# Kernel optimization log

Measured on AMD Instinct MI355X. Metric: run time of the kernel, lower is better.

## Reference

```python
import jax, jax.numpy as jnp
import numpy as np


def _lstm_dir(x, w_ih, w_hh, b_ih, b_hh, reverse):
    # x: [B, L, D]; w_ih: [4H, D]; w_hh: [4H, H]; PyTorch gate order i,f,g,o
    B = x.shape[0]
    H = w_hh.shape[1]
    h0 = jnp.zeros((B, H), x.dtype)

    def cell(carry, x_t):
        h, c = carry
        z = x_t @ w_ih.T + h @ w_hh.T + b_ih + b_hh
        i, f, g, o = jnp.split(z, 4, axis=-1)
        c = jax.nn.sigmoid(f) * c + jax.nn.sigmoid(i) * jnp.tanh(g)
        h = jax.nn.sigmoid(o) * jnp.tanh(c)
        return (h, c), h

    _, hs = jax.lax.scan(cell, (h0, h0), jnp.swapaxes(x, 0, 1), reverse=reverse)
    return jnp.swapaxes(hs, 0, 1)  # [B, L, H]


def setup_inputs() -> dict:
    key = jax.random.key(0)
    ks = jax.random.split(key, 16)
    B, L, V, D, H, E, A = 32, 128, 30000, 300, 128, 34, 36
    s = 0.05
    rn = lambda k, shape: jax.random.normal(k, shape, jnp.float32) * s
    return {
        "input_ids": jax.random.randint(ks[0], (B, L), 0, V),
        "emb": rn(ks[1], (V, D)),
        "w_ih_f": rn(ks[2], (4 * H, D)), "w_hh_f": rn(ks[3], (4 * H, H)),
        "b_ih_f": rn(ks[4], (4 * H,)), "b_hh_f": rn(ks[5], (4 * H,)),
        "w_ih_b": rn(ks[6], (4 * H, D)), "w_hh_b": rn(ks[7], (4 * H, H)),
        "b_ih_b": rn(ks[8], (4 * H,)), "b_hh_b": rn(ks[9], (4 * H,)),
        "event_w": rn(ks[10], (E, 2 * H)), "event_b": rn(ks[11], (E,)),
        "arg_w": rn(ks[12], (A, 4 * H + E - 1)), "arg_b": rn(ks[13], (A,)),
    }


def reference(input_ids, emb, w_ih_f, w_hh_f, b_ih_f, b_hh_f,
              w_ih_b, w_hh_b, b_ih_b, b_hh_b,
              event_w, event_b, arg_w, arg_b):
    # Eval mode: dropout is identity. No labels -> return (event_logits, arguments_logits).
    B, L = input_ids.shape
    E = event_b.shape[0]
    x = emb[input_ids]  # [B, L, D]
    h_f = _lstm_dir(x, w_ih_f, w_hh_f, b_ih_f, b_hh_f, False)
    h_b = _lstm_dir(x, w_ih_b, w_hh_b, b_ih_b, b_hh_b, True)
    hidden = jnp.concatenate([h_f, h_b], axis=-1)  # [B, L, 2H]
    col_range = jnp.arange(E - 1)
    g0 = jnp.zeros((B, L, E - 1), hidden.dtype)  # running g_trg_arg memory

    def step(g, h_i):  # h_i: [B, 2H] = trigger hidden state at timestep i
        ev_logit = h_i @ event_w.T + event_b  # [B, E]
        ev_pred = jnp.argmax(ev_logit, axis=-1)  # [B]
        trig = jnp.broadcast_to(h_i[:, None, :], hidden.shape)  # [B, L, 2H]
        ah = jnp.concatenate([hidden, trig, g], axis=-1)  # [B, L, 4H+E-1]
        arg_logit = ah @ arg_w.T + arg_b  # [B, L, A]
        arg_pred = jnp.argmax(arg_logit, axis=-1)  # [B, L]
        # Vectorized update_g_trg_arg: for batch items with ev_pred>0, set
        # column (ev_pred-1) to 1 wherever arg_pred>0, else keep previous value.
        mask_ev = ev_pred > 0  # [B]
        col = jnp.where(mask_ev, ev_pred - 1, 0)  # [B]
        onehot = (col[:, None] == col_range[None, :]) & mask_ev[:, None]  # [B, E-1]
        cond = onehot[:, None, :] & (arg_pred[:, :, None] > 0)  # [B, L, E-1]
        g = jnp.where(cond, jnp.ones((), g.dtype), g)
        return g, (ev_logit, arg_logit)

    _, (ev_logits, arg_logits) = jax.lax.scan(step, g0, jnp.swapaxes(hidden, 0, 1))
    event_logits = jnp.swapaxes(ev_logits, 0, 1)  # [B, L, E]
    arguments_logits = jnp.swapaxes(arg_logits, 0, 1)  # [B, L, L, A]
    return event_logits, arguments_logits
```

## Files before the change

### kernel.cpp

```cpp
#include <hip/hip_runtime.h>
#include <hip/hip_bf16.h>
#include <stdint.h>

#define B_  32
#define L_  128
#define D_  300
#define DP_ 304
#define H_  128
#define G_  512
#define E_  34
#define A_  36
#define M_  4096
#define NC_ 106
#define NCP 112
#define CH_ 8
#define NCH 16
#define LCH 8
#define NCHK (L_ / LCH)
#define BH_ 4

typedef float f2 __attribute__((ext_vector_type(2)));

__device__ __forceinline__ float sigf(float x){ return 1.0f / (1.0f + expf(-x)); }

__device__ __forceinline__ void bar_lds(){
    asm volatile("s_waitcnt lgkmcnt(0)" ::: "memory");
    __builtin_amdgcn_s_barrier();
    __builtin_amdgcn_sched_barrier(0);
}

__global__ void k_prep1(const float* __restrict__ wihf, const float* __restrict__ wihb,
                        float* __restrict__ WT){
    int k = blockIdx.x;
    int d = blockIdx.y;
    int n = threadIdx.x;
    const float* w = d ? wihb : wihf;
    WT[((size_t)d * DP_ + k) * G_ + n] = (k < D_) ? w[(size_t)n * D_ + k] : 0.0f;
}

__global__ void k_prep2(const float* __restrict__ evw, const float* __restrict__ evb,
                        const float* __restrict__ argw, const float* __restrict__ argb,
                        float* __restrict__ WcatT, float* __restrict__ biasv){
    int k = blockIdx.x;
    int n = threadIdx.x;
    if (n >= NCP) return;
    float v = 0.0f;
    if (n < E_)       v = evw[(size_t)n * 256 + k];
    else if (n < 70)  v = argw[(size_t)(n - 34) * 545 + k];
    else if (n < NC_) v = argw[(size_t)(n - 70) * 545 + 256 + k];
    WcatT[(size_t)k * NCP + n] = v;
    if (k == 0){
        float bv = 0.0f;
        if (n < E_) bv = evb[n];
        else if (n < 70) bv = argb[n - 34];
        biasv[n] = bv;
    }
}

__launch_bounds__(256)
__global__ void k_gemm1(const int* __restrict__ ids, const float* __restrict__ emb,
                        const float* __restrict__ WT,
                        const float* __restrict__ bihf, const float* __restrict__ bhhf,
                        const float* __restrict__ bihb, const float* __restrict__ bhhb,
                        float* __restrict__ XW){
    __shared__ __align__(16) float xs[DP_][8];
    int d  = blockIdx.y;
    int m0 = blockIdx.x * 8;
    int tid = threadIdx.x;
    for (int idx = tid; idx < 8 * DP_; idx += 256){
        int r = idx / DP_, k = idx % DP_;
        int id = ids[m0 + r];
        xs[k][r] = (k < D_) ? emb[(size_t)id * D_ + k] : 0.0f;
    }
    __syncthreads();
    int n0 = tid, n1 = tid + 256;
    const float* w0 = WT + (size_t)d * DP_ * G_ + n0;
    const float* w1 = WT + (size_t)d * DP_ * G_ + n1;
    const float4* xs4 = (const float4*)xs;
    float acc0[8] = {}, acc1[8] = {};
    #pragma unroll 2
    for (int k = 0; k < D_; k++){
        float wv0 = w0[(size_t)k * G_];
        float wv1 = w1[(size_t)k * G_];
        float4 xA = xs4[k * 2], xB = xs4[k * 2 + 1];
        acc0[0] += xA.x * wv0; acc0[1] += xA.y * wv0;
        acc0[2] += xA.z * wv0; acc0[3] += xA.w * wv0;
        acc0[4] += xB.x * wv0; acc0[5] += xB.y * wv0;
        acc0[6] += xB.z * wv0; acc0[7] += xB.w * wv0;
        acc1[0] += xA.x * wv1; acc1[1] += xA.y * wv1;
        acc1[2] += xA.z * wv1; acc1[3] += xA.w * wv1;
        acc1[4] += xB.x * wv1; acc1[5] += xB.y * wv1;
        acc1[6] += xB.z * wv1; acc1[7] += xB.w * wv1;
    }
    float bias0 = d ? (bihb[n0] + bhhb[n0]) : (bihf[n0] + bhhf[n0]);
    float bias1 = d ? (bihb[n1] + bhhb[n1]) : (bihf[n1] + bhhf[n1]);
    for (int r = 0; r < 8; r++){
        XW[((size_t)d * M_ + m0 + r) * G_ + n0] = acc0[r] + bias0;
        XW[((size_t)d * M_ + m0 + r) * G_ + n1] = acc1[r] + bias1;
    }
}

#define PF(XR, CHI)                                                             \
{                                                                               \
    if ((CHI) < NCHK){                                                          \
        _Pragma("unroll")                                                       \
        for (int j = 0; j < LCH; j++){                                          \
            int s_ = (CHI) * LCH + j;                                           \
            int t_ = d ? (L_ - 1 - s_) : s_;                                    \
            XR[j] = xwn[(size_t)t_ * G_];                                       \
        }                                                                       \
    }                                                                           \
}

#define STEP8(XR, CHI)                                                          \
{                                                                               \
    _Pragma("unroll")                                                           \
    for (int j = 0; j < LCH; j++){                                              \
        int s_ = (CHI) * LCH + j;                                               \
        f2 a01 = {0.f, 0.f}, a23 = {0.f, 0.f};                                  \
        const float4* hc = (const float4*)hbuf;                                 \
        _Pragma("unroll")                                                       \
        for (int q = 0; q < 32; q++){                                           \
            float4 hv = hc[q];                                                  \
            f2 h01 = {hv.x, hv.y}, h23 = {hv.z, hv.w};                          \
            a01 = __builtin_elementwise_fma(wp[2*q],   h01, a01);               \
            a23 = __builtin_elementwise_fma(wp[2*q+1], h23, a23);               \
        }                                                                       \
        float z = XR[j] + ((a01.x + a01.y) + (a23.x + a23.y));                  \
        float v = gate_g ? tanhf(z) : sigf(z);                                  \
        zbuf[n] = v;                                                            \
        bar_lds();                                                              \
        if (n < H_){                                                            \
            float F = zbuf[H_ + n], G = zbuf[2*H_ + n], O = zbuf[3*H_ + n];     \
            c = F * c + v * G;                                                  \
            float h = O * tanhf(c);                                             \
            hbuf[n] = h;                                                        \
            hist[(size_t)(s_) * H_ + n] = h;                                    \
        }                                                                       \
        bar_lds();                                                              \
    }                                                                           \
}

__launch_bounds__(512, 2)
__global__ void k_lstm(const float* __restrict__ XW, const float* __restrict__ whhf,
                       const float* __restrict__ whhb, float* __restrict__ Hid){
    __shared__ __align__(16) float hbuf[H_];
    __shared__ float zbuf[G_];
    __shared__ __align__(16) float hist[L_ * H_];
    int bid = blockIdx.x;
    int d = bid >> 5, b = bid & 31;
    int n = threadIdx.x;
    bool gate_g = ((n >> 7) == 2);
    const float* whh = d ? whhb : whhf;
    const f2* wr2 = (const f2*)(whh + (size_t)n * H_);
    f2 wp[64];
    #pragma unroll
    for (int q = 0; q < 64; q++) wp[q] = wr2[q];
    float c = 0.0f;
    if (n < H_) hbuf[n] = 0.0f;
    __syncthreads();
    const float* xwn = XW + ((size_t)d * M_ + (size_t)b * L_) * G_ + n;
    float xA[LCH], xB[LCH];
    PF(xA, 0)
    #pragma unroll 1
    for (int cp = 0; cp < NCHK / 2; cp++){
        PF(xB, 2 * cp + 1)
        STEP8(xA, 2 * cp)
        PF(xA, 2 * cp + 2)
        STEP8(xB, 2 * cp + 1)
    }
    const float4* hist4 = (const float4*)hist;
    #pragma unroll
    for (int q = 0; q < 8; q++){
        int idx = n + q * 512;
        int sl = idx >> 5, n4 = idx & 31;
        int t_ = d ? (L_ - 1 - sl) : sl;
        *(float4*)(Hid + ((size_t)b * L_ + t_) * 256 + d * H_ + n4 * 4) =
            hist4[(size_t)sl * 32 + n4];
    }
}

__launch_bounds__(128)
__global__ void k_heads2(const float* __restrict__ Hid, const float* __restrict__ WcatT,
                         const float* __restrict__ biasv,
                         float* __restrict__ out0, float* __restrict__ Base,
                         float* __restrict__ T2, int* __restrict__ Evcol){
    __shared__ __align__(16) float hsT[256][BH_];
    __shared__ float outs[BH_][NCP];
    int m0 = blockIdx.x * BH_;
    int tid = threadIdx.x;
    #pragma unroll
    for (int r = 0; r < BH_; r++){
        hsT[tid][r]       = Hid[(size_t)(m0 + r) * 256 + tid];
        hsT[tid + 128][r] = Hid[(size_t)(m0 + r) * 256 + 128 + tid];
    }
    __syncthreads();
    if (tid < NC_){
        float acc[BH_] = {};
        const float* wc = WcatT + tid;
        for (int k = 0; k < 256; k++){
            float wv = wc[(size_t)k * NCP];
            float4 h4 = *(const float4*)&hsT[k][0];
            acc[0] += h4.x * wv;
            acc[1] += h4.y * wv;
            acc[2] += h4.z * wv;
            acc[3] += h4.w * wv;
        }
        float bv = biasv[tid];
        #pragma unroll
        for (int r = 0; r < BH_; r++) outs[r][tid] = acc[r] + bv;
    }
    __syncthreads();
    for (int idx = tid; idx < BH_ * E_; idx += 128){
        int r = idx / E_, e = idx % E_;
        out0[(size_t)(m0 + r) * E_ + e] = outs[r][e];
    }
    for (int idx = tid; idx < BH_ * A_; idx += 128){
        int r = idx / A_, a = idx % A_;
        Base[(size_t)(m0 + r) * A_ + a] = outs[r][34 + a];
        T2[(size_t)(m0 + r) * A_ + a]   = outs[r][70 + a];
    }
    if (tid < BH_){
        float best = outs[tid][0]; int bi = 0;
        for (int e = 1; e < E_; e++){
            float v = outs[tid][e];
            if (v > best){ best = v; bi = e; }
        }
        Evcol[m0 + tid] = bi - 1;
    }
}

__launch_bounds__(128)
__global__ void k_scan1(const float* __restrict__ Base, const float* __restrict__ T2,
                        const int* __restrict__ Evcol, const float* __restrict__ argw,
                        float* __restrict__ Snap, uint64_t* __restrict__ MaskSnap){
    __shared__ float t2s[L_ * A_];
    __shared__ float wgs[33 * A_];
    __shared__ int   evc[L_];
    int b = blockIdx.x;
    int l = threadIdx.x;
    for (int idx = l; idx < L_ * A_; idx += 128)
        t2s[idx] = T2[(size_t)b * L_ * A_ + idx];
    for (int idx = l; idx < 33 * A_; idx += 128){
        int c = idx / A_, a = idx % A_;
        wgs[idx] = argw[(size_t)a * 545 + 512 + c];
    }
    evc[l] = Evcol[b * L_ + l];
    __syncthreads();
    float bg[A_];
    {
        const float* bp = Base + ((size_t)b * L_ + l) * A_;
        #pragma unroll
        for (int a = 0; a < A_; a++) bg[a] = bp[a];
    }
    uint64_t mask = 0;
    #pragma unroll 1
    for (int i = 0; i < L_; i++){
        if ((i & (CH_ - 1)) == 0){
            int ch = i >> 3;
            float* sp = Snap + (((size_t)b * NCH + ch) * L_ + l) * A_;
            #pragma unroll
            for (int a = 0; a < A_; a++) sp[a] = bg[a];
            MaskSnap[((size_t)b * NCH + ch) * L_ + l] = mask;
        }
        const float* tr = t2s + i * A_;
        float lg0 = bg[0] + tr[0];
        float m1  = bg[1] + tr[1];
        #pragma unroll
        for (int a = 2; a < A_; a++) m1 = fmaxf(m1, bg[a] + tr[a]);
        bool apos = m1 > lg0;
        int cc = evc[i];
        if (cc >= 0 && apos && !((mask >> cc) & 1ull)){
            mask |= 1ull << cc;
            const float* wc = wgs + cc * A_;
            #pragma unroll
            for (int a = 0; a < A_; a++) bg[a] += wc[a];
        }
    }
}

__launch_bounds__(128)
__global__ void k_scan2(const float* __restrict__ T2, const int* __restrict__ Evcol,
                        const float* __restrict__ argw,
                        const float* __restrict__ Snap, const uint64_t* __restrict__ MaskSnap,
                        float* __restrict__ argout){
    __shared__ float t2s[CH_ * A_];
    __shared__ float wgs[33 * A_];
    __shared__ int   evc[CH_];
    __shared__ float stg[L_ * 37];
    int ch = blockIdx.x;
    int b  = blockIdx.y;
    int l  = threadIdx.x;
    int i0 = ch * CH_;
    for (int idx = l; idx < CH_ * A_; idx += 128)
        t2s[idx] = T2[((size_t)b * L_ + i0) * A_ + idx];
    for (int idx = l; idx < 33 * A_; idx += 128){
        int c = idx / A_, a = idx % A_;
        wgs[idx] = argw[(size_t)a * 545 + 512 + c];
    }
    if (l < CH_) evc[l] = Evcol[b * L_ + i0 + l];
    __syncthreads();
    float bg[A_];
    {
        const float* sp = Snap + (((size_t)b * NCH + ch) * L_ + l) * A_;
        #pragma unroll
        for (int a = 0; a < A_; a++) bg[a] = sp[a];
    }
    uint64_t mask = MaskSnap[((size_t)b * NCH + ch) * L_ + l];
    #pragma unroll 1
    for (int s = 0; s < CH_; s++){
        int i = i0 + s;
        const float* tr = t2s + s * A_;
        float lg[A_];
        #pragma unroll
        for (int a = 0; a < A_; a++) lg[a] = bg[a] + tr[a];
        float m1 = lg[1];
        #pragma unroll
        for (int a = 2; a < A_; a++) m1 = fmaxf(m1, lg[a]);
        bool apos = m1 > lg[0];
        float* sr = stg + l * 37;
        #pragma unroll
        for (int a = 0; a < A_; a++) sr[a] = lg[a];
        int cc = evc[s];
        if (cc >= 0 && apos && !((mask >> cc) & 1ull)){
            mask |= 1ull << cc;
            const float* wc = wgs + cc * A_;
            #pragma unroll
            for (int a = 0; a < A_; a++) bg[a] += wc[a];
        }
        __syncthreads();
        float* op = argout + (((size_t)b * L_ + i) * L_) * A_;
        #pragma unroll
        for (int q = 0; q < 9; q++){
            int idx = l + q * 128;
            int row = idx / 9, c4 = idx % 9;
            const float* s0 = stg + row * 37 + c4 * 4;
            float4 v; v.x = s0[0]; v.y = s0[1]; v.z = s0[2]; v.w = s0[3];
            *(float4*)(op + (size_t)idx * 4) = v;
        }
        __syncthreads();
    }
}

extern "C" void kernel_launch(void* const* d_in, const int* in_sizes, int n_in,
                              void* d_out, int out_size, void* d_ws, size_t ws_size,
                              hipStream_t stream){
    const int*   ids  = (const int*)  d_in[0];
    const float* emb  = (const float*)d_in[1];
    const float* wihf = (const float*)d_in[2];
    const float* whhf = (const float*)d_in[3];
    const float* bihf = (const float*)d_in[4];
    const float* bhhf = (const float*)d_in[5];
    const float* wihb = (const float*)d_in[6];
    const float* whhb = (const float*)d_in[7];
    const float* bihb = (const float*)d_in[8];
    const float* bhhb = (const float*)d_in[9];
    const float* evw  = (const float*)d_in[10];
    const float* evb  = (const float*)d_in[11];
    const float* argw = (const float*)d_in[12];
    const float* argb = (const float*)d_in[13];

    float* out0   = (float*)d_out;
    float* argout = out0 + (size_t)M_ * E_;

    char* w = (char*)d_ws;
    float* WT    = (float*)w; w += (size_t)2 * DP_ * G_ * 4;
    float* XW    = (float*)w; w += (size_t)2 * M_ * G_ * 4;
    float* Hid   = (float*)w; w += (size_t)M_ * 256 * 4;
    float* WcatT = (float*)w; w += (size_t)256 * NCP * 4;
    float* biasv = (float*)w; w += (size_t)NCP * 4;
    float* Base  = (float*)w; w += (size_t)M_ * A_ * 4;
    float* T2    = (float*)w; w += (size_t)M_ * A_ * 4;
    int*   Evcol = (int*)w;   w += (size_t)M_ * 4;

    float*    Snap     = XW;
    uint64_t* MaskSnap = (uint64_t*)(XW + (size_t)B_ * NCH * L_ * A_);

    k_prep1<<<dim3(DP_, 2), 512, 0, stream>>>(wihf, wihb, WT);
    k_prep2<<<256, 128, 0, stream>>>(evw, evb, argw, argb, WcatT, biasv);
    k_gemm1<<<dim3(M_ / 8, 2), 256, 0, stream>>>(ids, emb, WT, bihf, bhhf, bihb, bhhb, XW);
    k_lstm<<<64, 512, 0, stream>>>(XW, whhf, whhb, Hid);
    k_heads2<<<M_ / BH_, 128, 0, stream>>>(Hid, WcatT, biasv, out0, Base, T2, Evcol);
    k_scan1<<<B_, 128, 0, stream>>>(Base, T2, Evcol, argw, Snap, MaskSnap);
    k_scan2<<<dim3(NCH, B_), 128, 0, stream>>>(T2, Evcol, argw, Snap, MaskSnap, argout);
}
```

Baseline: 367.5 us.

## Merge prep kernels, widen heads row tile, vectorize scan loads with float4

The two weight-prep kernels become one launch, which removes a kernel launch. The heads kernel now processes 8 rows per block instead of 4, so each loaded weight is reused across more rows and the block count is halved. The scan kernels read T2, Base and Snap with float4 loads and stores in both global and shared memory, which cuts instruction count. The merged prep kernel runs 512 threads for the WcatT part, where most threads sit idle, and the wider heads tile uses more registers.

```diff
diff --git a/kernel.cpp b/kernel.cpp
--- a/kernel.cpp
+++ b/kernel.cpp
@@ -17,7 +17,7 @@
 #define NCH 16
 #define LCH 8
 #define NCHK (L_ / LCH)
-#define BH_ 4
+#define BH_ 8
 
 typedef float f2 __attribute__((ext_vector_type(2)));
 
@@ -29,31 +29,33 @@
     __builtin_amdgcn_sched_barrier(0);
 }
 
-__global__ void k_prep1(const float* __restrict__ wihf, const float* __restrict__ wihb,
-                        float* __restrict__ WT){
-    int k = blockIdx.x;
-    int d = blockIdx.y;
-    int n = threadIdx.x;
-    const float* w = d ? wihb : wihf;
-    WT[((size_t)d * DP_ + k) * G_ + n] = (k < D_) ? w[(size_t)n * D_ + k] : 0.0f;
-}
-
-__global__ void k_prep2(const float* __restrict__ evw, const float* __restrict__ evb,
-                        const float* __restrict__ argw, const float* __restrict__ argb,
-                        float* __restrict__ WcatT, float* __restrict__ biasv){
-    int k = blockIdx.x;
-    int n = threadIdx.x;
-    if (n >= NCP) return;
-    float v = 0.0f;
-    if (n < E_)       v = evw[(size_t)n * 256 + k];
-    else if (n < 70)  v = argw[(size_t)(n - 34) * 545 + k];
-    else if (n < NC_) v = argw[(size_t)(n - 70) * 545 + 256 + k];
-    WcatT[(size_t)k * NCP + n] = v;
-    if (k == 0){
-        float bv = 0.0f;
-        if (n < E_) bv = evb[n];
-        else if (n < 70) bv = argb[n - 34];
-        biasv[n] = bv;
+__global__ void k_prep(const float* __restrict__ wihf, const float* __restrict__ wihb,
+                       float* __restrict__ WT,
+                       const float* __restrict__ evw, const float* __restrict__ evb,
+                       const float* __restrict__ argw, const float* __restrict__ argb,
+                       float* __restrict__ WcatT, float* __restrict__ biasv){
+    int bid = blockIdx.x;
+    int tid = threadIdx.x;
+    if (bid < 2 * DP_){
+        int d = bid / DP_, k = bid - d * DP_;
+        const float* w = d ? wihb : wihf;
+        WT[((size_t)d * DP_ + k) * G_ + tid] = (k < D_) ? w[(size_t)tid * D_ + k] : 0.0f;
+    } else {
+        int k = bid - 2 * DP_;
+        int n = tid;
+        if (n < NCP){
+            float v = 0.0f;
+            if (n < E_)       v = evw[(size_t)n * 256 + k];
+            else if (n < 70)  v = argw[(size_t)(n - 34) * 545 + k];
+            else if (n < NC_) v = argw[(size_t)(n - 70) * 545 + 256 + k];
+            WcatT[(size_t)k * NCP + n] = v;
+            if (k == 0){
+                float bv = 0.0f;
+                if (n < E_) bv = evb[n];
+                else if (n < 70) bv = argb[n - 34];
+                biasv[n] = bv;
+            }
+        }
     }
 }
 
@@ -200,11 +202,12 @@
         const float* wc = WcatT + tid;
         for (int k = 0; k < 256; k++){
             float wv = wc[(size_t)k * NCP];
-            float4 h4 = *(const float4*)&hsT[k][0];
-            acc[0] += h4.x * wv;
-            acc[1] += h4.y * wv;
-            acc[2] += h4.z * wv;
-            acc[3] += h4.w * wv;
+            float4 ha = *(const float4*)&hsT[k][0];
+            float4 hb = *(const float4*)&hsT[k][4];
+            acc[0] += ha.x * wv; acc[1] += ha.y * wv;
+            acc[2] += ha.z * wv; acc[3] += ha.w * wv;
+            acc[4] += hb.x * wv; acc[5] += hb.y * wv;
+            acc[6] += hb.z * wv; acc[7] += hb.w * wv;
         }
         float bv = biasv[tid];
         #pragma unroll
@@ -234,13 +237,13 @@
 __global__ void k_scan1(const float* __restrict__ Base, const float* __restrict__ T2,
                         const int* __restrict__ Evcol, const float* __restrict__ argw,
                         float* __restrict__ Snap, uint64_t* __restrict__ MaskSnap){
-    __shared__ float t2s[L_ * A_];
+    __shared__ __align__(16) float t2s[L_ * A_];
     __shared__ float wgs[33 * A_];
     __shared__ int   evc[L_];
     int b = blockIdx.x;
     int l = threadIdx.x;
-    for (int idx = l; idx < L_ * A_; idx += 128)
-        t2s[idx] = T2[(size_t)b * L_ * A_ + idx];
+    for (int idx = l; idx < L_ * A_ / 4; idx += 128)
+        *(float4*)(t2s + idx * 4) = *(const float4*)(T2 + (size_t)b * L_ * A_ + idx * 4);
     for (int idx = l; idx < 33 * A_; idx += 128){
         int c = idx / A_, a = idx % A_;
         wgs[idx] = argw[(size_t)a * 545 + 512 + c];
@@ -251,7 +254,10 @@
     {
         const float* bp = Base + ((size_t)b * L_ + l) * A_;
         #pragma unroll
-        for (int a = 0; a < A_; a++) bg[a] = bp[a];
+        for (int q = 0; q < 9; q++){
+            float4 v = *(const float4*)(bp + 4 * q);
+            bg[4*q] = v.x; bg[4*q+1] = v.y; bg[4*q+2] = v.z; bg[4*q+3] = v.w;
+        }
     }
     uint64_t mask = 0;
     #pragma unroll 1
@@ -260,14 +266,22 @@
             int ch = i >> 3;
             float* sp = Snap + (((size_t)b * NCH + ch) * L_ + l) * A_;
             #pragma unroll
-            for (int a = 0; a < A_; a++) sp[a] = bg[a];
+            for (int q = 0; q < 9; q++){
+                float4 v; v.x = bg[4*q]; v.y = bg[4*q+1]; v.z = bg[4*q+2]; v.w = bg[4*q+3];
+                *(float4*)(sp + 4 * q) = v;
+            }
             MaskSnap[((size_t)b * NCH + ch) * L_ + l] = mask;
         }
-        const float* tr = t2s + i * A_;
-        float lg0 = bg[0] + tr[0];
-        float m1  = bg[1] + tr[1];
-        #pragma unroll
-        for (int a = 2; a < A_; a++) m1 = fmaxf(m1, bg[a] + tr[a]);
+        float trv[A_];
+        #pragma unroll
+        for (int q = 0; q < 9; q++){
+            float4 v = *(const float4*)(t2s + i * A_ + 4 * q);
+            trv[4*q] = v.x; trv[4*q+1] = v.y; trv[4*q+2] = v.z; trv[4*q+3] = v.w;
+        }
+        float lg0 = bg[0] + trv[0];
+        float m1  = bg[1] + trv[1];
+        #pragma unroll
+        for (int a = 2; a < A_; a++) m1 = fmaxf(m1, bg[a] + trv[a]);
         bool apos = m1 > lg0;
         int cc = evc[i];
         if (cc >= 0 && apos && !((mask >> cc) & 1ull)){
@@ -284,7 +298,7 @@
                         const float* __restrict__ argw,
                         const float* __restrict__ Snap, const uint64_t* __restrict__ MaskSnap,
                         float* __restrict__ argout){
-    __shared__ float t2s[CH_ * A_];
+    __shared__ __align__(16) float t2s[CH_ * A_];
     __shared__ float wgs[33 * A_];
     __shared__ int   evc[CH_];
     __shared__ float stg[L_ * 37];
@@ -292,8 +306,9 @@
     int b  = blockIdx.y;
     int l  = threadIdx.x;
     int i0 = ch * CH_;
-    for (int idx = l; idx < CH_ * A_; idx += 128)
-        t2s[idx] = T2[((size_t)b * L_ + i0) * A_ + idx];
+    for (int idx = l; idx < CH_ * A_ / 4; idx += 128)
+        *(float4*)(t2s + idx * 4) =
+            *(const float4*)(T2 + ((size_t)b * L_ + i0) * A_ + idx * 4);
     for (int idx = l; idx < 33 * A_; idx += 128){
         int c = idx / A_, a = idx % A_;
         wgs[idx] = argw[(size_t)a * 545 + 512 + c];
@@ -304,16 +319,24 @@
     {
         const float* sp = Snap + (((size_t)b * NCH + ch) * L_ + l) * A_;
         #pragma unroll
-        for (int a = 0; a < A_; a++) bg[a] = sp[a];
+        for (int q = 0; q < 9; q++){
+            float4 v = *(const float4*)(sp + 4 * q);
+            bg[4*q] = v.x; bg[4*q+1] = v.y; bg[4*q+2] = v.z; bg[4*q+3] = v.w;
+        }
     }
     uint64_t mask = MaskSnap[((size_t)b * NCH + ch) * L_ + l];
     #pragma unroll 1
     for (int s = 0; s < CH_; s++){
         int i = i0 + s;
-        const float* tr = t2s + s * A_;
+        float trv[A_];
+        #pragma unroll
+        for (int q = 0; q < 9; q++){
+            float4 v = *(const float4*)(t2s + s * A_ + 4 * q);
+            trv[4*q] = v.x; trv[4*q+1] = v.y; trv[4*q+2] = v.z; trv[4*q+3] = v.w;
+        }
         float lg[A_];
         #pragma unroll
-        for (int a = 0; a < A_; a++) lg[a] = bg[a] + tr[a];
+        for (int a = 0; a < A_; a++) lg[a] = bg[a] + trv[a];
         float m1 = lg[1];
         #pragma unroll
         for (int a = 2; a < A_; a++) m1 = fmaxf(m1, lg[a]);
@@ -376,8 +399,8 @@
     float*    Snap     = XW;
     uint64_t* MaskSnap = (uint64_t*)(XW + (size_t)B_ * NCH * L_ * A_);
 
-    k_prep1<<<dim3(DP_, 2), 512, 0, stream>>>(wihf, wihb, WT);
-    k_prep2<<<256, 128, 0, stream>>>(evw, evb, argw, argb, WcatT, biasv);
+    k_prep<<<2 * DP_ + 256, 512, 0, stream>>>(wihf, wihb, WT, evw, evb, argw, argb,
+                                              WcatT, biasv);
     k_gemm1<<<dim3(M_ / 8, 2), 256, 0, stream>>>(ids, emb, WT, bihf, bhhf, bihb, bhhb, XW);
     k_lstm<<<64, 512, 0, stream>>>(XW, whhf, whhb, Hid);
     k_heads2<<<M_ / BH_, 128, 0, stream>>>(Hid, WcatT, biasv, out0, Base, T2, Evcol);
```

After: 359.7 us. 2.1% less time.
